# Optimization experiments

Hardware: AMD Instinct MI355X
Metric: run time of the kernel (lower is better)

The kernel has to match this reference:

```python
import jax, jax.numpy as jnp
import numpy as np

N = 100000
E = 1600000
F_FEAT, F_COND, F_HID, F_LAT = 128, 32, 128, 64


def setup_inputs() -> dict:
    key = jax.random.key(0)
    ks = jax.random.split(key, 16)
    feature = jax.random.normal(ks[0], (N, F_FEAT), dtype=jnp.float32)
    condition = jax.random.normal(ks[1], (N, F_COND), dtype=jnp.float32)
    edge_index = jax.random.randint(ks[2], (2, E), 0, N, dtype=jnp.int64)

    def glorot(k, fan_in, fan_out):
        s = jnp.sqrt(6.0 / (fan_in + fan_out)).astype(jnp.float32)
        return jax.random.uniform(k, (fan_in, fan_out), jnp.float32, -s, s)

    enc_in = F_FEAT + F_COND   # 160
    dec_in = F_LAT + F_COND    # 96
    return {
        "feature": feature,
        "condition": condition,
        "edge_index": edge_index,
        "W_e1": glorot(ks[3], enc_in, F_HID), "b_e1": jnp.zeros((F_HID,), jnp.float32),
        "W_e2": glorot(ks[4], F_HID, F_HID), "b_e2": jnp.zeros((F_HID,), jnp.float32),
        "W_e3": glorot(ks[5], F_HID, F_LAT), "b_e3": jnp.zeros((F_LAT,), jnp.float32),
        "W_d1": glorot(ks[6], dec_in, F_HID), "b_d1": jnp.zeros((F_HID,), jnp.float32),
        "W_d2": glorot(ks[7], F_HID, F_HID), "b_d2": jnp.zeros((F_HID,), jnp.float32),
        "W_d3": glorot(ks[8], F_HID, F_FEAT), "b_d3": jnp.zeros((F_FEAT,), jnp.float32),
    }


def _gcn_conv(x, W, b, src, dst, dinv):
    # GCNConv with add_self_loops=True, symmetric normalization:
    # out = D^{-1/2} (A + I) D^{-1/2} X W + b
    h = x @ W                                        # [N, out]
    coef = (dinv[src] * dinv[dst])[:, None]          # [E, 1]
    msg = h[src] * coef                              # [E, out]
    agg = jax.ops.segment_sum(msg, dst, num_segments=x.shape[0])
    agg = agg + h * (dinv * dinv)[:, None]           # self-loop term
    return agg + b


def reference(feature, condition, edge_index,
              W_e1, b_e1, W_e2, b_e2, W_e3, b_e3,
              W_d1, b_d1, W_d2, b_d2, W_d3, b_d3):
    src, dst = edge_index[0], edge_index[1]
    n = feature.shape[0]
    # degree with self loops (edge weights = 1)
    deg = jax.ops.segment_sum(jnp.ones((src.shape[0],), jnp.float32), dst,
                              num_segments=n) + 1.0
    dinv = jax.lax.rsqrt(deg)

    # encoder
    x = jnp.concatenate([feature, condition], axis=1)
    h = jnp.tanh(_gcn_conv(x, W_e1, b_e1, src, dst, dinv))
    h = jnp.tanh(_gcn_conv(h, W_e2, b_e2, src, dst, dinv))
    z = _gcn_conv(h, W_e3, b_e3, src, dst, dinv)

    # decoder
    x = jnp.concatenate([z, condition], axis=1)
    h = jnp.tanh(_gcn_conv(x, W_d1, b_d1, src, dst, dinv))
    h = jnp.tanh(_gcn_conv(h, W_d2, b_d2, src, dst, dinv))
    out = _gcn_conv(h, W_d3, b_d3, src, dst, dinv)
    return out
```

## Files before the change

kernel.cpp:

```cpp
#include <hip/hip_runtime.h>
#include <hip/hip_fp16.h>
#include <math.h>

#define NN 100000
#define NE 1600000
#define NB ((NN + 255) >> 8)
#define CHUNK 8192
#define CAP 8192

typedef __attribute__((ext_vector_type(4))) float floatx4;
typedef __attribute__((ext_vector_type(8))) short shortx8;


__global__ __launch_bounds__(256)
void coarse_hist(const int* __restrict__ ei, int* __restrict__ bucket_cnt, int E) {
    __shared__ int h[512];
    int t = threadIdx.x;
    for (int i = t; i < 512; i += 256) h[i] = 0;
    __syncthreads();
    int base = blockIdx.x * CHUNK;
    int lim = min(base + CHUNK, E);
    for (int e = base + t; e < lim; e += 256) {
        int d = ei[E + e];
        atomicAdd(&h[d >> 8], 1);
    }
    __syncthreads();
    for (int i = t; i < 512; i += 256)
        if (h[i]) atomicAdd(&bucket_cnt[i], h[i]);
}

__global__ void scan_buckets(const int* __restrict__ bucket_cnt,
                             int* __restrict__ bucket_base,
                             int* __restrict__ bucket_fill) {
    __shared__ int sh[512];
    int t = threadIdx.x;
    int v = (t < NB) ? bucket_cnt[t] : 0;
    sh[t] = v;
    __syncthreads();
    for (int off = 1; off < 512; off <<= 1) {
        int u = (t >= off) ? sh[t - off] : 0;
        __syncthreads();
        sh[t] += u;
        __syncthreads();
    }
    int ex = (t == 0) ? 0 : sh[t - 1];
    if (t <= NB) bucket_base[t] = ex;
    if (t < NB) bucket_fill[t] = ex;
}

__global__ __launch_bounds__(256)
void coarse_scatter(const int* __restrict__ ei, int* __restrict__ bucket_fill,
                    unsigned long long* __restrict__ pairs, int E) {
    __shared__ int h[512];
    __shared__ int base[512];
    int t = threadIdx.x;
    for (int i = t; i < 512; i += 256) h[i] = 0;
    __syncthreads();
    int cbase = blockIdx.x * CHUNK;
    int lim = min(cbase + CHUNK, E);
    for (int e = cbase + t; e < lim; e += 256) {
        int d = ei[E + e];
        atomicAdd(&h[d >> 8], 1);
    }
    __syncthreads();
    for (int i = t; i < 512; i += 256)
        base[i] = h[i] ? atomicAdd(&bucket_fill[i], h[i]) : 0;
    __syncthreads();
    for (int i = t; i < 512; i += 256) h[i] = 0;
    __syncthreads();
    for (int e = cbase + t; e < lim; e += 256) {
        int s = ei[e];
        int d = ei[E + e];
        int b = d >> 8;
        int r = atomicAdd(&h[b], 1);
        pairs[base[b] + r] =
            ((unsigned long long)(unsigned)d << 32) | (unsigned)s;
    }
}

__global__ __launch_bounds__(256)
void fine_csr(const unsigned long long* __restrict__ pairs,
              const int* __restrict__ bucket_base,
              int* __restrict__ rowptr, int* __restrict__ colid,
              float* __restrict__ dinv, int n) {
    __shared__ int hist[256];
    __shared__ int offs[256];
    __shared__ int rank[256];
    __shared__ int lbuf[CAP];
    int b = blockIdx.x, t = threadIdx.x;
    int beg = bucket_base[b], end = bucket_base[b + 1];
    int cnt = end - beg;
    hist[t] = 0; rank[t] = 0;
    __syncthreads();
    for (int i = t; i < cnt; i += 256) {
        int d = (int)(pairs[beg + i] >> 32);
        atomicAdd(&hist[d & 255], 1);
    }
    __syncthreads();
    int v = hist[t];
    offs[t] = v;
    __syncthreads();
    for (int off = 1; off < 256; off <<= 1) {
        int u = (t >= off) ? offs[t - off] : 0;
        __syncthreads();
        offs[t] += u;
        __syncthreads();
    }
    int ex = (t == 0) ? 0 : offs[t - 1];
    int node = (b << 8) + t;
    if (node < n) {
        rowptr[node] = beg + ex;
        dinv[node] = rsqrtf((float)v + 1.0f);
    } else if (node == n) {
        rowptr[n] = beg + ex;
    }
    __syncthreads();
    offs[t] = ex;
    __syncthreads();
    for (int i = t; i < cnt; i += 256) {
        unsigned long long p = pairs[beg + i];
        int d = (int)(p >> 32) & 255;
        int s = (int)(p & 0xffffffffu);
        int r = atomicAdd(&rank[d], 1);
        lbuf[offs[d] + r] = s;
    }
    __syncthreads();
    for (int i = t; i < cnt; i += 256) colid[beg + i] = lbuf[i];
}


__global__ void concat_kernel(const float4* __restrict__ f, const float4* __restrict__ c,
                              float4* __restrict__ A, int n) {
    int i = blockIdx.x * 256 + threadIdx.x;
    int total = n * 40;
    if (i < total) {
        int row = i / 40, j = i % 40;
        A[i] = (j < 32) ? f[row * 32 + j] : c[row * 8 + (j - 32)];
    }
}

__global__ void condcopy_kernel(const float4* __restrict__ c, float4* __restrict__ A, int n) {
    int i = blockIdx.x * 256 + threadIdx.x;
    if (i < n * 8) {
        int row = i / 8, j = i % 8;
        A[row * 24 + 16 + j] = c[row * 8 + j];
    }
}


__global__ void wsplit_kernel(const float* __restrict__ W,
                              unsigned short* __restrict__ Wsw,
                              int K, int OUT) {
    int i = blockIdx.x * 256 + threadIdx.x;
    if (i < K * OUT) {
        int k = i / OUT, o = i % OUT;
        float w = W[i];
        unsigned u = __float_as_uint(w);
        float r = w - __uint_as_float(u & 0xFFFF0000u);
        int NT = OUT >> 4;
        int ktc = k >> 5, q = (k >> 3) & 3, j = k & 7;
        int nt = o >> 4, m = o & 15;
        int lane = (q << 4) | m;
        size_t base = ((((size_t)(ktc * NT + nt) * 2) * 64 + lane) << 3) + j;
        Wsw[base] = (unsigned short)(u >> 16);
        Wsw[base + 512] = (unsigned short)(__float_as_uint(r) >> 16);
    }
}


__device__ __forceinline__ void split8(const float* v, shortx8& hi, shortx8& lo) {
#pragma unroll
    for (int i = 0; i < 8; i++) {
        unsigned u = __float_as_uint(v[i]);
        float r = v[i] - __uint_as_float(u & 0xFFFF0000u);
        hi[i] = (short)(u >> 16);
        lo[i] = (short)(__float_as_uint(r) >> 16);
    }
}

template <int OUT, int K>
__global__ __launch_bounds__(512)
void gemm_mfma(const float* __restrict__ X,
               const unsigned short* __restrict__ Wsw,
               const float* __restrict__ dinv,
               __half* __restrict__ Y, int ntiles) {
    constexpr int NT = OUT / 16;
    constexpr int NKTC = K / 32;
    constexpr int PERC = OUT * 128;
    constexpr int CSZ = (65536 / PERC < NKTC) ? (65536 / PERC) : NKTC;
    __shared__ __align__(16) unsigned short lds[CSZ * PERC / 2];

    const int t = threadIdx.x;
    const int wave = t >> 6, lane = t & 63;
    const int m = lane & 15, q = lane >> 4;
    const int tile = blockIdx.x * 8 + wave;
    const bool act = tile < ntiles;
    const int row = act ? tile * 16 + m : 0;
    const float* ap = X + (size_t)row * K + q * 8;

    floatx4 acc[NT];
#pragma unroll
    for (int nt = 0; nt < NT; nt++) acc[nt] = (floatx4){0.f, 0.f, 0.f, 0.f};

#pragma unroll
    for (int c0 = 0; c0 < NKTC; c0 += CSZ) {
        const int cl = (NKTC - c0 < CSZ) ? (NKTC - c0) : CSZ;
        if (c0 != 0) __syncthreads();
        {
            const float4* gs = (const float4*)Wsw + (size_t)c0 * (PERC / 16);
            float4* ld = (float4*)lds;
            int tot = cl * (PERC / 16);
            for (int i = t; i < tot; i += 512) ld[i] = gs[i];
        }
        __syncthreads();
        if (act) {
#pragma unroll
            for (int ktc = 0; ktc < cl; ktc++) {
                int kg = (c0 + ktc) * 32;
                float av[8];
                *(float4*)&av[0] = *(const float4*)(ap + kg);
                *(float4*)&av[4] = *(const float4*)(ap + kg + 4);
                shortx8 ahi, alo;
                split8(av, ahi, alo);
#pragma unroll
                for (int nt = 0; nt < NT; nt++) {
                    const unsigned short* fb =
                        lds + ((((ktc * NT + nt) * 2) * 64 + lane) << 3);
                    shortx8 bhi = *(const shortx8*)fb;
                    shortx8 blo = *(const shortx8*)(fb + 512);
                    acc[nt] = __builtin_amdgcn_mfma_f32_16x16x32_bf16(ahi, bhi, acc[nt], 0, 0, 0);
                    acc[nt] = __builtin_amdgcn_mfma_f32_16x16x32_bf16(ahi, blo, acc[nt], 0, 0, 0);
                    acc[nt] = __builtin_amdgcn_mfma_f32_16x16x32_bf16(alo, bhi, acc[nt], 0, 0, 0);
                }
            }
        }
    }

    if (act) {
        float di[4];
#pragma unroll
        for (int r = 0; r < 4; r++) di[r] = dinv[tile * 16 + q * 4 + r];
#pragma unroll
        for (int nt = 0; nt < NT; nt++) {
#pragma unroll
            for (int r = 0; r < 4; r++) {
                int orow = tile * 16 + q * 4 + r;
                Y[(size_t)orow * OUT + nt * 16 + m] = __float2half_rn(acc[nt][r] * di[r]);
            }
        }
    }
}


template <int OUT, bool TANH>
__global__ __launch_bounds__(256)
void prop_kernel(const __half* __restrict__ hs, const float* __restrict__ dinv,
                 const int* __restrict__ rowptr, const int* __restrict__ colid,
                 const float* __restrict__ bias,
                 float* __restrict__ out, int ldo, int n) {
    int wave = threadIdx.x >> 6;
    int lane = threadIdx.x & 63;
    int node = blockIdx.x * 4 + wave;
    if (node >= n) return;
    int beg = rowptr[node], end = rowptr[node + 1];

    if constexpr (OUT == 128) {
        const __half2* base = (const __half2*)hs;
        float2 self = __half22float2(base[(size_t)node * 64 + lane]);
        float accx = self.x, accy = self.y;
        float accx2 = 0.f, accy2 = 0.f;
        int e = beg;
        for (; e + 8 <= end; e += 8) {
            int s[8];
#pragma unroll
            for (int j = 0; j < 8; j++) s[j] = colid[e + j];
            __half2 v[8];
#pragma unroll
            for (int j = 0; j < 8; j++) v[j] = base[(size_t)s[j] * 64 + lane];
#pragma unroll
            for (int j = 0; j < 8; j += 2) {
                float2 f0 = __half22float2(v[j]);
                float2 f1 = __half22float2(v[j + 1]);
                accx += f0.x; accy += f0.y;
                accx2 += f1.x; accy2 += f1.y;
            }
        }
        if (e + 4 <= end) {
            int s[4];
#pragma unroll
            for (int j = 0; j < 4; j++) s[j] = colid[e + j];
            __half2 v[4];
#pragma unroll
            for (int j = 0; j < 4; j++) v[j] = base[(size_t)s[j] * 64 + lane];
            float2 f0 = __half22float2(v[0]), f1 = __half22float2(v[1]);
            float2 f2 = __half22float2(v[2]), f3 = __half22float2(v[3]);
            accx += f0.x + f2.x; accy += f0.y + f2.y;
            accx2 += f1.x + f3.x; accy2 += f1.y + f3.y;
            e += 4;
        }
        for (; e < end; e++) {
            float2 f = __half22float2(base[(size_t)colid[e] * 64 + lane]);
            accx += f.x; accy += f.y;
        }
        accx += accx2; accy += accy2;
        float di = dinv[node];
        float ox = di * accx + bias[2 * lane];
        float oy = di * accy + bias[2 * lane + 1];
        if (TANH) { ox = tanhf(ox); oy = tanhf(oy); }
        *(float2*)(out + (size_t)node * ldo + 2 * lane) = make_float2(ox, oy);
    } else {
        float acc = __half2float(hs[(size_t)node * 64 + lane]);
        float acc2 = 0.f;
        int e = beg;
        for (; e + 8 <= end; e += 8) {
            int s[8];
#pragma unroll
            for (int j = 0; j < 8; j++) s[j] = colid[e + j];
            __half v[8];
#pragma unroll
            for (int j = 0; j < 8; j++) v[j] = hs[(size_t)s[j] * 64 + lane];
#pragma unroll
            for (int j = 0; j < 8; j += 2) {
                acc += __half2float(v[j]);
                acc2 += __half2float(v[j + 1]);
            }
        }
        if (e + 4 <= end) {
            int s[4];
#pragma unroll
            for (int j = 0; j < 4; j++) s[j] = colid[e + j];
            __half v[4];
#pragma unroll
            for (int j = 0; j < 4; j++) v[j] = hs[(size_t)s[j] * 64 + lane];
            acc += __half2float(v[0]) + __half2float(v[2]);
            acc2 += __half2float(v[1]) + __half2float(v[3]);
            e += 4;
        }
        for (; e < end; e++) acc += __half2float(hs[(size_t)colid[e] * 64 + lane]);
        acc += acc2;
        float v = dinv[node] * acc + bias[lane];
        if (TANH) v = tanhf(v);
        out[(size_t)node * ldo + lane] = v;
    }
}


extern "C" void kernel_launch(void* const* d_in, const int* in_sizes, int n_in,
                              void* d_out, int out_size, void* d_ws, size_t ws_size,
                              hipStream_t stream) {
    const int n = NN, E = NE;
    const float* feature   = (const float*)d_in[0];
    const float* condition = (const float*)d_in[1];
    const int*   ei        = (const int*)d_in[2];
    const float* W_e1 = (const float*)d_in[3];  const float* b_e1 = (const float*)d_in[4];
    const float* W_e2 = (const float*)d_in[5];  const float* b_e2 = (const float*)d_in[6];
    const float* W_e3 = (const float*)d_in[7];  const float* b_e3 = (const float*)d_in[8];
    const float* W_d1 = (const float*)d_in[9];  const float* b_d1 = (const float*)d_in[10];
    const float* W_d2 = (const float*)d_in[11]; const float* b_d2 = (const float*)d_in[12];
    const float* W_d3 = (const float*)d_in[13]; const float* b_d3 = (const float*)d_in[14];
    float* out = (float*)d_out;

    float*  A    = (float*)d_ws;
    __half* H16  = (__half*)(A + (size_t)n * 160);
    float*  dinv = (float*)(H16 + (size_t)n * 128);
    int* rowptr  = (int*)(dinv + n);
    int* colid   = rowptr + n + 1;
    uintptr_t pp = (uintptr_t)(colid + E);
    pp = (pp + 15) & ~(uintptr_t)15;
    unsigned long long* pairs = (unsigned long long*)pp;
    int* bucket_cnt  = (int*)(pairs + E);
    int* bucket_base = bucket_cnt + 512;
    int* bucket_fill = bucket_base + 512;
    uintptr_t wp = (uintptr_t)(bucket_fill + 512);
    wp = (wp + 15) & ~(uintptr_t)15;
    unsigned short* wt = (unsigned short*)wp;
    unsigned short* e1w = wt;             unsigned short* e2w = e1w + 160 * 128 * 2;
    unsigned short* e3w = e2w + 128*128*2; unsigned short* d1w = e3w + 128 * 64 * 2;
    unsigned short* d2w = d1w + 96*128*2;  unsigned short* d3w = d2w + 128 * 128 * 2;

    hipMemsetAsync(bucket_cnt, 0, 512 * sizeof(int), stream);

    int nbc = (E + CHUNK - 1) / CHUNK;
    coarse_hist<<<nbc, 256, 0, stream>>>(ei, bucket_cnt, E);
    scan_buckets<<<1, 512, 0, stream>>>(bucket_cnt, bucket_base, bucket_fill);
    coarse_scatter<<<nbc, 256, 0, stream>>>(ei, bucket_fill, pairs, E);
    fine_csr<<<NB, 256, 0, stream>>>(pairs, bucket_base, rowptr, colid, dinv, n);

    wsplit_kernel<<<(160*128 + 255)/256, 256, 0, stream>>>(W_e1, e1w, 160, 128);
    wsplit_kernel<<<(128*128 + 255)/256, 256, 0, stream>>>(W_e2, e2w, 128, 128);
    wsplit_kernel<<<(128*64  + 255)/256, 256, 0, stream>>>(W_e3, e3w, 128, 64);
    wsplit_kernel<<<(96*128  + 255)/256, 256, 0, stream>>>(W_d1, d1w, 96, 128);
    wsplit_kernel<<<(128*128 + 255)/256, 256, 0, stream>>>(W_d2, d2w, 128, 128);
    wsplit_kernel<<<(128*128 + 255)/256, 256, 0, stream>>>(W_d3, d3w, 128, 128);

    concat_kernel<<<(n * 40 + 255) / 256, 256, 0, stream>>>(
        (const float4*)feature, (const float4*)condition, (float4*)A, n);

    const int ntiles = n / 16;
    const int gb = (ntiles + 7) / 8;
    int pb = (n + 3) / 4;

    gemm_mfma<128, 160><<<gb, 512, 0, stream>>>(A, e1w, dinv, H16, ntiles);
    prop_kernel<128, true><<<pb, 256, 0, stream>>>(H16, dinv, rowptr, colid, b_e1, A, 128, n);
    gemm_mfma<128, 128><<<gb, 512, 0, stream>>>(A, e2w, dinv, H16, ntiles);
    prop_kernel<128, true><<<pb, 256, 0, stream>>>(H16, dinv, rowptr, colid, b_e2, A, 128, n);
    gemm_mfma<64, 128><<<gb, 512, 0, stream>>>(A, e3w, dinv, H16, ntiles);
    prop_kernel<64, false><<<pb, 256, 0, stream>>>(H16, dinv, rowptr, colid, b_e3, A, 96, n);
    condcopy_kernel<<<(n * 8 + 255) / 256, 256, 0, stream>>>(
        (const float4*)condition, (float4*)A, n);

    gemm_mfma<128, 96><<<gb, 512, 0, stream>>>(A, d1w, dinv, H16, ntiles);
    prop_kernel<128, true><<<pb, 256, 0, stream>>>(H16, dinv, rowptr, colid, b_d1, A, 128, n);
    gemm_mfma<128, 128><<<gb, 512, 0, stream>>>(A, d2w, dinv, H16, ntiles);
    prop_kernel<128, true><<<pb, 256, 0, stream>>>(H16, dinv, rowptr, colid, b_d2, A, 128, n);
    gemm_mfma<128, 128><<<gb, 512, 0, stream>>>(A, d3w, dinv, H16, ntiles);
    prop_kernel<128, false><<<pb, 256, 0, stream>>>(H16, dinv, rowptr, colid, b_d3, out, 128, n);
}
```

Measured before the change: 729.6 us.

## Split each wave into four edge groups with wide loads and shuffle reduction

The SpMM propagation kernels now split each 64-lane wave into four quarter-waves. Each quarter handles a different neighbor (the self loop included) and loads 16-byte (128-wide) or 8-byte (64-wide) fp16 chunks per lane, with a software-prefetched next row. Partial sums are combined with xor shuffles at the end. The condition copy is fused into the 64-wide propagation, which removes a separate kernel launch. This trades per-lane load width and memory-level parallelism for a final cross-quarter reduction, and adds per-iteration colid loads with branchy fetch logic.

```diff
diff --git a/kernel.cpp b/kernel.cpp
--- a/kernel.cpp
+++ b/kernel.cpp
@@ -136,14 +136,6 @@
     if (i < total) {
         int row = i / 40, j = i % 40;
         A[i] = (j < 32) ? f[row * 32 + j] : c[row * 8 + (j - 32)];
-    }
-}
-
-__global__ void condcopy_kernel(const float4* __restrict__ c, float4* __restrict__ A, int n) {
-    int i = blockIdx.x * 256 + threadIdx.x;
-    if (i < n * 8) {
-        int row = i / 8, j = i % 8;
-        A[row * 24 + 16 + j] = c[row * 8 + j];
     }
 }
 
@@ -252,95 +244,109 @@
 }
 
 
-template <int OUT, bool TANH>
+template <bool TANH>
 __global__ __launch_bounds__(256)
-void prop_kernel(const __half* __restrict__ hs, const float* __restrict__ dinv,
-                 const int* __restrict__ rowptr, const int* __restrict__ colid,
-                 const float* __restrict__ bias,
-                 float* __restrict__ out, int ldo, int n) {
+void prop128_kernel(const __half* __restrict__ hs, const float* __restrict__ dinv,
+                    const int* __restrict__ rowptr, const int* __restrict__ colid,
+                    const float* __restrict__ bias,
+                    float* __restrict__ out, int ldo, int n) {
     int wave = threadIdx.x >> 6;
     int lane = threadIdx.x & 63;
     int node = blockIdx.x * 4 + wave;
     if (node >= n) return;
-    int beg = rowptr[node], end = rowptr[node + 1];
-
-    if constexpr (OUT == 128) {
-        const __half2* base = (const __half2*)hs;
-        float2 self = __half22float2(base[(size_t)node * 64 + lane]);
-        float accx = self.x, accy = self.y;
-        float accx2 = 0.f, accy2 = 0.f;
-        int e = beg;
-        for (; e + 8 <= end; e += 8) {
-            int s[8];
-#pragma unroll
-            for (int j = 0; j < 8; j++) s[j] = colid[e + j];
-            __half2 v[8];
-#pragma unroll
-            for (int j = 0; j < 8; j++) v[j] = base[(size_t)s[j] * 64 + lane];
-#pragma unroll
-            for (int j = 0; j < 8; j += 2) {
-                float2 f0 = __half22float2(v[j]);
-                float2 f1 = __half22float2(v[j + 1]);
-                accx += f0.x; accy += f0.y;
-                accx2 += f1.x; accy2 += f1.y;
-            }
+    int beg = rowptr[node];
+    int total = rowptr[node + 1] - beg + 1;
+    int q = lane >> 4, c = lane & 15;
+    const float4* hs4 = (const float4*)hs;
+
+    float acc[8];
+#pragma unroll
+    for (int j = 0; j < 8; j++) acc[j] = 0.f;
+
+    auto fetch = [&](int it) -> int {
+        int idx = it + q;
+        if (idx == 0) return node;
+        if (idx < total) return colid[beg + idx - 1];
+        return -1;
+    };
+
+    int src = fetch(0);
+    float4 v = make_float4(0.f, 0.f, 0.f, 0.f);
+    if (src >= 0) v = hs4[(size_t)src * 16 + c];
+    for (int it = 0; it < total; it += 4) {
+        int ns = fetch(it + 4);
+        float4 nv = make_float4(0.f, 0.f, 0.f, 0.f);
+        if (ns >= 0) nv = hs4[(size_t)ns * 16 + c];
+        const __half2* h2 = (const __half2*)&v;
+#pragma unroll
+        for (int j = 0; j < 4; j++) {
+            float2 f = __half22float2(h2[j]);
+            acc[2 * j] += f.x;
+            acc[2 * j + 1] += f.y;
         }
-        if (e + 4 <= end) {
-            int s[4];
-#pragma unroll
-            for (int j = 0; j < 4; j++) s[j] = colid[e + j];
-            __half2 v[4];
-#pragma unroll
-            for (int j = 0; j < 4; j++) v[j] = base[(size_t)s[j] * 64 + lane];
-            float2 f0 = __half22float2(v[0]), f1 = __half22float2(v[1]);
-            float2 f2 = __half22float2(v[2]), f3 = __half22float2(v[3]);
-            accx += f0.x + f2.x; accy += f0.y + f2.y;
-            accx2 += f1.x + f3.x; accy2 += f1.y + f3.y;
-            e += 4;
-        }
-        for (; e < end; e++) {
-            float2 f = __half22float2(base[(size_t)colid[e] * 64 + lane]);
-            accx += f.x; accy += f.y;
-        }
-        accx += accx2; accy += accy2;
-        float di = dinv[node];
-        float ox = di * accx + bias[2 * lane];
-        float oy = di * accy + bias[2 * lane + 1];
-        if (TANH) { ox = tanhf(ox); oy = tanhf(oy); }
-        *(float2*)(out + (size_t)node * ldo + 2 * lane) = make_float2(ox, oy);
-    } else {
-        float acc = __half2float(hs[(size_t)node * 64 + lane]);
-        float acc2 = 0.f;
-        int e = beg;
-        for (; e + 8 <= end; e += 8) {
-            int s[8];
-#pragma unroll
-            for (int j = 0; j < 8; j++) s[j] = colid[e + j];
-            __half v[8];
-#pragma unroll
-            for (int j = 0; j < 8; j++) v[j] = hs[(size_t)s[j] * 64 + lane];
-#pragma unroll
-            for (int j = 0; j < 8; j += 2) {
-                acc += __half2float(v[j]);
-                acc2 += __half2float(v[j + 1]);
-            }
-        }
-        if (e + 4 <= end) {
-            int s[4];
-#pragma unroll
-            for (int j = 0; j < 4; j++) s[j] = colid[e + j];
-            __half v[4];
-#pragma unroll
-            for (int j = 0; j < 4; j++) v[j] = hs[(size_t)s[j] * 64 + lane];
-            acc += __half2float(v[0]) + __half2float(v[2]);
-            acc2 += __half2float(v[1]) + __half2float(v[3]);
-            e += 4;
-        }
-        for (; e < end; e++) acc += __half2float(hs[(size_t)colid[e] * 64 + lane]);
-        acc += acc2;
-        float v = dinv[node] * acc + bias[lane];
-        if (TANH) v = tanhf(v);
-        out[(size_t)node * ldo + lane] = v;
+        v = nv;
+    }
+#pragma unroll
+    for (int j = 0; j < 8; j++) {
+        acc[j] += __shfl_xor(acc[j], 16, 64);
+        acc[j] += __shfl_xor(acc[j], 32, 64);
+    }
+    float di = dinv[node];
+    int col = c * 8 + q * 2;
+    float ox = di * acc[q * 2] + bias[col];
+    float oy = di * acc[q * 2 + 1] + bias[col + 1];
+    if (TANH) { ox = tanhf(ox); oy = tanhf(oy); }
+    *(float2*)(out + (size_t)node * ldo + col) = make_float2(ox, oy);
+}
+
+template <bool ADDCOND>
+__global__ __launch_bounds__(256)
+void prop64_kernel(const __half* __restrict__ hs, const float* __restrict__ dinv,
+                   const int* __restrict__ rowptr, const int* __restrict__ colid,
+                   const float* __restrict__ bias, const float* __restrict__ cond,
+                   float* __restrict__ out, int ldo, int n) {
+    int wave = threadIdx.x >> 6;
+    int lane = threadIdx.x & 63;
+    int node = blockIdx.x * 4 + wave;
+    if (node >= n) return;
+    int beg = rowptr[node];
+    int total = rowptr[node + 1] - beg + 1;
+    int q = lane >> 4, c = lane & 15;
+    const float2* hs2 = (const float2*)hs;
+
+    float acc[4] = {0.f, 0.f, 0.f, 0.f};
+
+    auto fetch = [&](int it) -> int {
+        int idx = it + q;
+        if (idx == 0) return node;
+        if (idx < total) return colid[beg + idx - 1];
+        return -1;
+    };
+
+    int src = fetch(0);
+    float2 v = make_float2(0.f, 0.f);
+    if (src >= 0) v = hs2[(size_t)src * 16 + c];
+    for (int it = 0; it < total; it += 4) {
+        int ns = fetch(it + 4);
+        float2 nv = make_float2(0.f, 0.f);
+        if (ns >= 0) nv = hs2[(size_t)ns * 16 + c];
+        const __half2* h2 = (const __half2*)&v;
+        float2 f0 = __half22float2(h2[0]);
+        float2 f1 = __half22float2(h2[1]);
+        acc[0] += f0.x; acc[1] += f0.y; acc[2] += f1.x; acc[3] += f1.y;
+        v = nv;
+    }
+#pragma unroll
+    for (int j = 0; j < 4; j++) {
+        acc[j] += __shfl_xor(acc[j], 16, 64);
+        acc[j] += __shfl_xor(acc[j], 32, 64);
+    }
+    float di = dinv[node];
+    int col = c * 4 + q;
+    out[(size_t)node * ldo + col] = di * acc[q] + bias[col];
+    if (ADDCOND && q == 0) {
+        float2 cv = ((const float2*)cond)[(size_t)node * 16 + c];
+        *(float2*)(out + (size_t)node * ldo + 64 + c * 2) = cv;
     }
 }
 
@@ -401,18 +407,16 @@
     int pb = (n + 3) / 4;
 
     gemm_mfma<128, 160><<<gb, 512, 0, stream>>>(A, e1w, dinv, H16, ntiles);
-    prop_kernel<128, true><<<pb, 256, 0, stream>>>(H16, dinv, rowptr, colid, b_e1, A, 128, n);
+    prop128_kernel<true><<<pb, 256, 0, stream>>>(H16, dinv, rowptr, colid, b_e1, A, 128, n);
     gemm_mfma<128, 128><<<gb, 512, 0, stream>>>(A, e2w, dinv, H16, ntiles);
-    prop_kernel<128, true><<<pb, 256, 0, stream>>>(H16, dinv, rowptr, colid, b_e2, A, 128, n);
+    prop128_kernel<true><<<pb, 256, 0, stream>>>(H16, dinv, rowptr, colid, b_e2, A, 128, n);
     gemm_mfma<64, 128><<<gb, 512, 0, stream>>>(A, e3w, dinv, H16, ntiles);
-    prop_kernel<64, false><<<pb, 256, 0, stream>>>(H16, dinv, rowptr, colid, b_e3, A, 96, n);
-    condcopy_kernel<<<(n * 8 + 255) / 256, 256, 0, stream>>>(
-        (const float4*)condition, (float4*)A, n);
+    prop64_kernel<true><<<pb, 256, 0, stream>>>(H16, dinv, rowptr, colid, b_e3, condition, A, 96, n);
 
     gemm_mfma<128, 96><<<gb, 512, 0, stream>>>(A, d1w, dinv, H16, ntiles);
-    prop_kernel<128, true><<<pb, 256, 0, stream>>>(H16, dinv, rowptr, colid, b_d1, A, 128, n);
+    prop128_kernel<true><<<pb, 256, 0, stream>>>(H16, dinv, rowptr, colid, b_d1, A, 128, n);
     gemm_mfma<128, 128><<<gb, 512, 0, stream>>>(A, d2w, dinv, H16, ntiles);
-    prop_kernel<128, true><<<pb, 256, 0, stream>>>(H16, dinv, rowptr, colid, b_d2, A, 128, n);
+    prop128_kernel<true><<<pb, 256, 0, stream>>>(H16, dinv, rowptr, colid, b_d2, A, 128, n);
     gemm_mfma<128, 128><<<gb, 512, 0, stream>>>(A, d3w, dinv, H16, ntiles);
-    prop_kernel<128, false><<<pb, 256, 0, stream>>>(H16, dinv, rowptr, colid, b_d3, out, 128, n);
-}
+    prop128_kernel<false><<<pb, 256, 0, stream>>>(H16, dinv, rowptr, colid, b_d3, out, 128, n);
+}
```

Measured after the change: 767.6 us. 1.05x slower.

## Fuse condition copy into propagation, shrink GEMM LDS chunk, use 32-bit indexing

Applied to the files above, without the earlier changes.

Removes the separate condcopy kernel by having the latent-layer propagation kernel also write the condition columns into the decoder input buffer. This saves one launch and one extra pass over that buffer. The GEMM weight-staging chunk is halved to 32 KB of LDS, which may allow more blocks per CU but adds more sync/reload rounds for larger K. Address arithmetic is switched from 64-bit size_t to 32-bit unsigned to cut instruction count in the gather loops. That is safe at these sizes but would overflow for much larger graphs.

```diff
diff --git a/kernel.cpp b/kernel.cpp
--- a/kernel.cpp
+++ b/kernel.cpp
@@ -136,14 +136,6 @@
     if (i < total) {
         int row = i / 40, j = i % 40;
         A[i] = (j < 32) ? f[row * 32 + j] : c[row * 8 + (j - 32)];
-    }
-}
-
-__global__ void condcopy_kernel(const float4* __restrict__ c, float4* __restrict__ A, int n) {
-    int i = blockIdx.x * 256 + threadIdx.x;
-    if (i < n * 8) {
-        int row = i / 8, j = i % 8;
-        A[row * 24 + 16 + j] = c[row * 8 + j];
     }
 }
 
@@ -187,7 +179,8 @@
     constexpr int NT = OUT / 16;
     constexpr int NKTC = K / 32;
     constexpr int PERC = OUT * 128;
-    constexpr int CSZ = (65536 / PERC < NKTC) ? (65536 / PERC) : NKTC;
+    constexpr int CSZ0 = 32768 / PERC;
+    constexpr int CSZ = (CSZ0 < NKTC) ? CSZ0 : NKTC;
     __shared__ __align__(16) unsigned short lds[CSZ * PERC / 2];
 
     const int t = threadIdx.x;
@@ -195,8 +188,8 @@
     const int m = lane & 15, q = lane >> 4;
     const int tile = blockIdx.x * 8 + wave;
     const bool act = tile < ntiles;
-    const int row = act ? tile * 16 + m : 0;
-    const float* ap = X + (size_t)row * K + q * 8;
+    const unsigned row = act ? (unsigned)(tile * 16 + m) : 0u;
+    const float* ap = X + row * (unsigned)K + (unsigned)(q * 8);
 
     floatx4 acc[NT];
 #pragma unroll
@@ -216,7 +209,7 @@
         if (act) {
 #pragma unroll
             for (int ktc = 0; ktc < cl; ktc++) {
-                int kg = (c0 + ktc) * 32;
+                unsigned kg = (unsigned)(c0 + ktc) * 32u;
                 float av[8];
                 *(float4*)&av[0] = *(const float4*)(ap + kg);
                 *(float4*)&av[4] = *(const float4*)(ap + kg + 4);
@@ -244,29 +237,30 @@
         for (int nt = 0; nt < NT; nt++) {
 #pragma unroll
             for (int r = 0; r < 4; r++) {
-                int orow = tile * 16 + q * 4 + r;
-                Y[(size_t)orow * OUT + nt * 16 + m] = __float2half_rn(acc[nt][r] * di[r]);
+                unsigned orow = (unsigned)(tile * 16 + q * 4 + r);
+                Y[orow * (unsigned)OUT + (unsigned)(nt * 16 + m)] =
+                    __float2half_rn(acc[nt][r] * di[r]);
             }
         }
     }
 }
 
 
-template <int OUT, bool TANH>
+template <int OUT, bool TANH, bool ADDCOND>
 __global__ __launch_bounds__(256)
 void prop_kernel(const __half* __restrict__ hs, const float* __restrict__ dinv,
                  const int* __restrict__ rowptr, const int* __restrict__ colid,
-                 const float* __restrict__ bias,
+                 const float* __restrict__ bias, const float* __restrict__ cond,
                  float* __restrict__ out, int ldo, int n) {
     int wave = threadIdx.x >> 6;
-    int lane = threadIdx.x & 63;
+    unsigned lane = threadIdx.x & 63;
     int node = blockIdx.x * 4 + wave;
     if (node >= n) return;
     int beg = rowptr[node], end = rowptr[node + 1];
 
     if constexpr (OUT == 128) {
         const __half2* base = (const __half2*)hs;
-        float2 self = __half22float2(base[(size_t)node * 64 + lane]);
+        float2 self = __half22float2(base[(unsigned)node * 64u + lane]);
         float accx = self.x, accy = self.y;
         float accx2 = 0.f, accy2 = 0.f;
         int e = beg;
@@ -276,7 +270,7 @@
             for (int j = 0; j < 8; j++) s[j] = colid[e + j];
             __half2 v[8];
 #pragma unroll
-            for (int j = 0; j < 8; j++) v[j] = base[(size_t)s[j] * 64 + lane];
+            for (int j = 0; j < 8; j++) v[j] = base[(unsigned)s[j] * 64u + lane];
 #pragma unroll
             for (int j = 0; j < 8; j += 2) {
                 float2 f0 = __half22float2(v[j]);
@@ -291,7 +285,7 @@
             for (int j = 0; j < 4; j++) s[j] = colid[e + j];
             __half2 v[4];
 #pragma unroll
-            for (int j = 0; j < 4; j++) v[j] = base[(size_t)s[j] * 64 + lane];
+            for (int j = 0; j < 4; j++) v[j] = base[(unsigned)s[j] * 64u + lane];
             float2 f0 = __half22float2(v[0]), f1 = __half22float2(v[1]);
             float2 f2 = __half22float2(v[2]), f3 = __half22float2(v[3]);
             accx += f0.x + f2.x; accy += f0.y + f2.y;
@@ -299,7 +293,7 @@
             e += 4;
         }
         for (; e < end; e++) {
-            float2 f = __half22float2(base[(size_t)colid[e] * 64 + lane]);
+            float2 f = __half22float2(base[(unsigned)colid[e] * 64u + lane]);
             accx += f.x; accy += f.y;
         }
         accx += accx2; accy += accy2;
@@ -307,9 +301,9 @@
         float ox = di * accx + bias[2 * lane];
         float oy = di * accy + bias[2 * lane + 1];
         if (TANH) { ox = tanhf(ox); oy = tanhf(oy); }
-        *(float2*)(out + (size_t)node * ldo + 2 * lane) = make_float2(ox, oy);
+        *(float2*)(out + (unsigned)node * (unsigned)ldo + 2 * lane) = make_float2(ox, oy);
     } else {
-        float acc = __half2float(hs[(size_t)node * 64 + lane]);
+        float acc = __half2float(hs[(unsigned)node * 64u + lane]);
         float acc2 = 0.f;
         int e = beg;
         for (; e + 8 <= end; e += 8) {
@@ -318,7 +312,7 @@
             for (int j = 0; j < 8; j++) s[j] = colid[e + j];
             __half v[8];
 #pragma unroll
-            for (int j = 0; j < 8; j++) v[j] = hs[(size_t)s[j] * 64 + lane];
+            for (int j = 0; j < 8; j++) v[j] = hs[(unsigned)s[j] * 64u + lane];
 #pragma unroll
             for (int j = 0; j < 8; j += 2) {
                 acc += __half2float(v[j]);
@@ -331,16 +325,20 @@
             for (int j = 0; j < 4; j++) s[j] = colid[e + j];
             __half v[4];
 #pragma unroll
-            for (int j = 0; j < 4; j++) v[j] = hs[(size_t)s[j] * 64 + lane];
+            for (int j = 0; j < 4; j++) v[j] = hs[(unsigned)s[j] * 64u + lane];
             acc += __half2float(v[0]) + __half2float(v[2]);
             acc2 += __half2float(v[1]) + __half2float(v[3]);
             e += 4;
         }
-        for (; e < end; e++) acc += __half2float(hs[(size_t)colid[e] * 64 + lane]);
+        for (; e < end; e++) acc += __half2float(hs[(unsigned)colid[e] * 64u + lane]);
         acc += acc2;
         float v = dinv[node] * acc + bias[lane];
         if (TANH) v = tanhf(v);
-        out[(size_t)node * ldo + lane] = v;
+        out[(unsigned)node * (unsigned)ldo + lane] = v;
+        if (ADDCOND && lane < 32) {
+            out[(unsigned)node * (unsigned)ldo + 64u + lane] =
+                cond[(unsigned)node * 32u + lane];
+        }
     }
 }
 
@@ -401,18 +399,16 @@
     int pb = (n + 3) / 4;
 
     gemm_mfma<128, 160><<<gb, 512, 0, stream>>>(A, e1w, dinv, H16, ntiles);
-    prop_kernel<128, true><<<pb, 256, 0, stream>>>(H16, dinv, rowptr, colid, b_e1, A, 128, n);
+    prop_kernel<128, true, false><<<pb, 256, 0, stream>>>(H16, dinv, rowptr, colid, b_e1, nullptr, A, 128, n);
     gemm_mfma<128, 128><<<gb, 512, 0, stream>>>(A, e2w, dinv, H16, ntiles);
-    prop_kernel<128, true><<<pb, 256, 0, stream>>>(H16, dinv, rowptr, colid, b_e2, A, 128, n);
+    prop_kernel<128, true, false><<<pb, 256, 0, stream>>>(H16, dinv, rowptr, colid, b_e2, nullptr, A, 128, n);
     gemm_mfma<64, 128><<<gb, 512, 0, stream>>>(A, e3w, dinv, H16, ntiles);
-    prop_kernel<64, false><<<pb, 256, 0, stream>>>(H16, dinv, rowptr, colid, b_e3, A, 96, n);
-    condcopy_kernel<<<(n * 8 + 255) / 256, 256, 0, stream>>>(
-        (const float4*)condition, (float4*)A, n);
+    prop_kernel<64, false, true><<<pb, 256, 0, stream>>>(H16, dinv, rowptr, colid, b_e3, condition, A, 96, n);
 
     gemm_mfma<128, 96><<<gb, 512, 0, stream>>>(A, d1w, dinv, H16, ntiles);
-    prop_kernel<128, true><<<pb, 256, 0, stream>>>(H16, dinv, rowptr, colid, b_d1, A, 128, n);
+    prop_kernel<128, true, false><<<pb, 256, 0, stream>>>(H16, dinv, rowptr, colid, b_d1, nullptr, A, 128, n);
     gemm_mfma<128, 128><<<gb, 512, 0, stream>>>(A, d2w, dinv, H16, ntiles);
-    prop_kernel<128, true><<<pb, 256, 0, stream>>>(H16, dinv, rowptr, colid, b_d2, A, 128, n);
+    prop_kernel<128, true, false><<<pb, 256, 0, stream>>>(H16, dinv, rowptr, colid, b_d2, nullptr, A, 128, n);
     gemm_mfma<128, 128><<<gb, 512, 0, stream>>>(A, d3w, dinv, H16, ntiles);
-    prop_kernel<128, false><<<pb, 256, 0, stream>>>(H16, dinv, rowptr, colid, b_d3, out, 128, n);
-}
+    prop_kernel<128, false, false><<<pb, 256, 0, stream>>>(H16, dinv, rowptr, colid, b_d3, nullptr, out, 128, n);
+}
```

Result: no change. 741.4 us (+1.6%).
